# Kernel optimization log

Hardware: AMD Instinct MI355X
Metric: run time of the kernel (lower is better)

Reference implementation:

```python
import jax, jax.numpy as jnp
import numpy as np

N, E, B = 100000, 1200000, 512
IN_DIM, HID, K, NCLS = 64, 64, 3, 10


def setup_inputs() -> dict:
    key = jax.random.key(0)
    ks = jax.random.split(key, 10)
    features = jax.random.normal(ks[0], (N, IN_DIM), jnp.float32)
    edge_src = jax.random.randint(ks[1], (E,), 0, N)
    edge_dst = jax.random.randint(ks[2], (E,), 0, N)
    graph_ids = jnp.sort(jax.random.randint(ks[3], (N,), 0, B))
    s1 = float(1.0 / np.sqrt(IN_DIM))
    W1 = jax.random.uniform(ks[4], (IN_DIM, HID), jnp.float32, -s1, s1)
    b1 = jnp.zeros((HID,), jnp.float32)
    s2 = float(1.0 / np.sqrt(HID))
    W2 = jax.random.uniform(ks[5], (HID, HID), jnp.float32, -s2, s2)
    b2 = jnp.zeros((HID,), jnp.float32)
    s3 = float(1.0 / np.sqrt(HID * 3))
    cw = jax.random.uniform(ks[6], (HID, HID, 3), jnp.float32, -s3, s3)
    cb = jax.random.uniform(ks[7], (HID,), jnp.float32, -s3, s3)
    Wc = jax.random.uniform(ks[8], (HID, NCLS), jnp.float32, -s2, s2)
    bc = jax.random.uniform(ks[9], (NCLS,), jnp.float32, -s2, s2)
    return dict(features=features, edge_src=edge_src, edge_dst=edge_dst,
                graph_ids=graph_ids, num_graphs=B,
                W1=W1, b1=b1, W2=W2, b2=b2, cw=cw, cb=cb, Wc=Wc, bc=bc)


def graph_conv(h, src, dst, W, b, n_nodes):
    # DGL GraphConv, norm='both', allow_zero_in_degree (degrees clamped to 1)
    ones = jnp.ones((src.shape[0],), h.dtype)
    out_deg = jnp.zeros((n_nodes,), h.dtype).at[src].add(ones)
    in_deg = jnp.zeros((n_nodes,), h.dtype).at[dst].add(ones)
    norm_s = jax.lax.rsqrt(jnp.clip(out_deg, 1.0, None))
    norm_d = jax.lax.rsqrt(jnp.clip(in_deg, 1.0, None))
    m = (h * norm_s[:, None]) @ W  # weight first; math identical to agg-first
    agg = jnp.zeros((n_nodes, W.shape[1]), h.dtype).at[dst].add(m[src])
    return agg * norm_d[:, None] + b


def sort_pool(h, gid, num_graphs, k):
    # DGL SortPooling: sort each node's features ascending along feature dim,
    # then take top-k nodes per graph by last feature value (descending),
    # zero-padding graphs with < k nodes. Output [num_graphs, k*D].
    hs = jnp.sort(h, axis=-1)
    key = hs[:, -1]
    order = jnp.lexsort((-key, gid))  # gid asc, key desc
    gid_s = gid[order]
    hs_s = hs[order]
    n = gid.shape[0]
    start = jnp.full((num_graphs,), n).at[gid_s].min(jnp.arange(n))
    rank = jnp.arange(n) - start[gid_s]  # within-graph rank by key desc
    mask = rank < k
    slot = gid_s * k + jnp.clip(rank, 0, k - 1)
    out = jnp.zeros((num_graphs * k, hs.shape[-1]), h.dtype).at[slot].add(
        jnp.where(mask[:, None], hs_s, jnp.zeros((), h.dtype)))
    return out.reshape(num_graphs, k * hs.shape[-1])


def reference(features, edge_src, edge_dst, graph_ids, num_graphs,
              W1, b1, W2, b2, cw, cb, Wc, bc):
    n = features.shape[0]
    h = jax.nn.relu(graph_conv(features, edge_src, edge_dst, W1, b1, n))
    h = jax.nn.relu(graph_conv(h, edge_src, edge_dst, W2, b2, n))
    p = sort_pool(h, graph_ids, num_graphs, K)          # [B, K*HID]
    x = p.reshape(num_graphs, HID, K)                    # faithful torch reshape
    # Conv1d(kernel=3, stride=1) on length-3 input -> length-1 output
    y = jax.nn.relu(jnp.einsum('bct,oct->bo', x, cw) + cb)
    return y @ Wc + bc
```

## Files before the change

kernel.cpp:

```cpp
#include <hip/hip_runtime.h>
#include <hip/hip_bf16.h>


#define PART_H 50176
#define QPART_H (PART_H / 4)
#define PART_F 25088
#define QUART_F (PART_F / 4)
#define MCH  64

__global__ void __launch_bounds__(256) k_histgemm(
    const int* __restrict__ esrc, const int* __restrict__ edst,
    unsigned char* __restrict__ hd, unsigned char* __restrict__ hs,
    const float* __restrict__ in, const float* __restrict__ W,
    float* __restrict__ mout, int N, int E, int PH, int histBlocks) {
  __shared__ float smem[12800];
  const int t = threadIdx.x;
  if (blockIdx.x < histBlocks) {
    unsigned int* lc = (unsigned int*)smem;
    const int b = blockIdx.x;
    const int half = PH * MCH;
    const int a = b / half;
    const int r = b % half;
    const int p = r % PH;
    const int m = r / PH;
    const int* __restrict__ arr = a ? esrc : edst;
    unsigned char* __restrict__ outp = a ? hs : hd;
    const int base = p * PART_H;
    const int lim = min(PART_H, N - base);
    for (int i = t; i < QPART_H; i += 256) lc[i] = 0u;
    __syncthreads();
    const long long cb = (long long)m * E / MCH;
    const long long ce = (long long)(m + 1) * E / MCH;
    const long long a0 = min((cb + 3) & ~3LL, ce);
    const long long nv = (ce - a0) >> 2;
    for (long long e = cb + t; e < a0; e += 256) {
      int d = arr[e] - base;
      if ((unsigned)d < (unsigned)lim) atomicAdd(&lc[d >> 2], 1u << ((d & 3) * 8));
    }
    const int4* __restrict__ a4p = (const int4*)(arr + a0);
    for (long long i = t; i < nv; i += 256) {
      int4 v4 = a4p[i];
      int d;
      d = v4.x - base; if ((unsigned)d < (unsigned)lim) atomicAdd(&lc[d >> 2], 1u << ((d & 3) * 8));
      d = v4.y - base; if ((unsigned)d < (unsigned)lim) atomicAdd(&lc[d >> 2], 1u << ((d & 3) * 8));
      d = v4.z - base; if ((unsigned)d < (unsigned)lim) atomicAdd(&lc[d >> 2], 1u << ((d & 3) * 8));
      d = v4.w - base; if ((unsigned)d < (unsigned)lim) atomicAdd(&lc[d >> 2], 1u << ((d & 3) * 8));
    }
    for (long long e = a0 + (nv << 2) + t; e < ce; e += 256) {
      int d = arr[e] - base;
      if ((unsigned)d < (unsigned)lim) atomicAdd(&lc[d >> 2], 1u << ((d & 3) * 8));
    }
    __syncthreads();
    unsigned char* slice = outp + ((size_t)p * MCH + m) * PART_H;
    for (int i = t; i < lim; i += 256)
      slice[i] = (unsigned char)((lc[i >> 2] >> ((i & 3) * 8)) & 0xffu);
  } else {
    float* Wl = smem;
    float* Ac = smem + 4096;
    const int ch = (t & 7) * 8;
    const int nb = (t >> 3) * 4;
    for (int i = t; i < 1024; i += 256)
      ((float4*)Wl)[i] = ((const float4*)W)[i];
    const int gb = blockIdx.x - histBlocks;
    const int ng = gridDim.x - histBlocks;
    const int NT = (N + 127) >> 7;
    for (int tile = gb; tile < NT; tile += ng) {
      const int vbase = tile << 7;
      __syncthreads();
      for (int i = t; i < 2048; i += 256) {
        const int r = i >> 4;
        const int c = (i & 15) * 4;
        const int v = vbase + r;
        float4 val = make_float4(0.f, 0.f, 0.f, 0.f);
        if (v < N) val = *(const float4*)(in + (size_t)v * 64 + c);
        Ac[(c + 0) * 136 + r] = val.x;
        Ac[(c + 1) * 136 + r] = val.y;
        Ac[(c + 2) * 136 + r] = val.z;
        Ac[(c + 3) * 136 + r] = val.w;
      }
      __syncthreads();
      float acc[4][8];
#pragma unroll
      for (int j = 0; j < 4; ++j)
#pragma unroll
        for (int c = 0; c < 8; ++c) acc[j][c] = 0.f;
      for (int k = 0; k < 64; k += 4) {
#pragma unroll
        for (int kk = 0; kk < 4; ++kk) {
          const float4 aa = *(const float4*)&Ac[(k + kk) * 136 + nb];
          const float4 w0 = *(const float4*)&Wl[(k + kk) * 64 + ch];
          const float4 w1 = *(const float4*)&Wl[(k + kk) * 64 + ch + 4];
          const float an[4] = {aa.x, aa.y, aa.z, aa.w};
          const float wn[8] = {w0.x, w0.y, w0.z, w0.w, w1.x, w1.y, w1.z, w1.w};
#pragma unroll
          for (int j = 0; j < 4; ++j)
#pragma unroll
            for (int c = 0; c < 8; ++c)
              acc[j][c] = fmaf(an[j], wn[c], acc[j][c]);
        }
      }
#pragma unroll
      for (int j = 0; j < 4; ++j) {
        const int v = vbase + nb + j;
        if (v < N) {
          float4 o0, o1;
          o0.x = acc[j][0]; o0.y = acc[j][1]; o0.z = acc[j][2]; o0.w = acc[j][3];
          o1.x = acc[j][4]; o1.y = acc[j][5]; o1.z = acc[j][6]; o1.w = acc[j][7];
          *(float4*)(mout + (size_t)v * 64 + ch)     = o0;
          *(float4*)(mout + (size_t)v * 64 + ch + 4) = o1;
        }
      }
    }
  }
}

__global__ void __launch_bounds__(256) k_offscan(
    unsigned char* __restrict__ hd, const unsigned char* __restrict__ hs,
    int* __restrict__ deg_d, float* __restrict__ norm_s, float* __restrict__ norm_d,
    int* __restrict__ gstart, int* __restrict__ rowptr, int* __restrict__ bsum,
    int B, int N) {
  __shared__ int sums[256];
  const int t = threadIdx.x;
  const int v0 = blockIdx.x * 2048 + t * 8;
#pragma unroll
  for (int j = 0; j < 8; ++j)
    if (v0 + j < B) gstart[v0 + j] = 0x7f7f7f7f;
  unsigned long long drun = 0ull, stot = 0ull;
  if (v0 < N) {
    const size_t rb = (size_t)(v0 / PART_H) * MCH * PART_H + (size_t)(v0 % PART_H);
    unsigned long long* __restrict__ hd8 = (unsigned long long*)(hd + rb);
    const unsigned long long* __restrict__ hs8 = (const unsigned long long*)(hs + rb);
    const size_t st8 = PART_H / 8;
#pragma unroll 8
    for (int m = 0; m < MCH; ++m) {
      unsigned long long c = hd8[(size_t)m * st8];
      hd8[(size_t)m * st8] = drun;
      drun += c;
      stot += hs8[(size_t)m * st8];
    }
  }
  int loc[8];
  int tot = 0;
#pragma unroll
  for (int j = 0; j < 8; ++j) {
    const int v = v0 + j;
    const int dg = (v < N) ? (int)((drun >> (8 * j)) & 0xffull) : 0;
    loc[j] = tot;
    tot += dg;
    if (v < N) {
      deg_d[v] = dg;
      norm_d[v] = rsqrtf((float)max(dg, 1));
      const int so = (int)((stot >> (8 * j)) & 0xffull);
      norm_s[v] = rsqrtf((float)max(so, 1));
    }
  }
  sums[t] = tot;
  __syncthreads();
  for (int off = 1; off < 256; off <<= 1) {
    int x = (t >= off) ? sums[t - off] : 0;
    __syncthreads();
    sums[t] += x;
    __syncthreads();
  }
  int excl = (t == 0) ? 0 : sums[t - 1];
#pragma unroll
  for (int j = 0; j < 8; ++j) {
    const int v = v0 + j;
    if (v < N) rowptr[v] = excl + loc[j];
  }
  if (t == 255) bsum[blockIdx.x] = sums[255];
}

__global__ void k_scan2(int* __restrict__ bsum, int nb) {
  int lane = threadIdx.x;
  int v = (lane < nb) ? bsum[lane] : 0;
  int inc = v;
#pragma unroll
  for (int off = 1; off < 64; off <<= 1) {
    int o = __shfl_up(inc, off, 64);
    if (lane >= off) inc += o;
  }
  if (lane < nb) bsum[lane] = inc - v;
}

__global__ void k_fill2(const int* __restrict__ esrc, const int* __restrict__ edst,
                        const unsigned char* __restrict__ hd, const int* __restrict__ rowptr,
                        const int* __restrict__ bsum, int* __restrict__ csr,
                        int N, int E, int PF) {
  __shared__ unsigned int cur4[QUART_F];
  const int b = blockIdx.x;
  const int p = b % PF;
  const int m = b / PF;
  const int base = p * PART_F;
  const int lim = min(PART_F, N - base);
  const unsigned char* slice = hd + ((size_t)(p >> 1) * MCH + m) * PART_H
                                  + (size_t)(p & 1) * PART_F;
  const unsigned int* slice4 = (const unsigned int*)slice;
  for (int i = threadIdx.x; i < QUART_F; i += blockDim.x) cur4[i] = slice4[i];
  __syncthreads();
  const int* __restrict__ rp = rowptr + base;
  const long long cb = (long long)m * E / MCH;
  const long long ce = (long long)(m + 1) * E / MCH;
  const long long a0 = min((cb + 3) & ~3LL, ce);
  const long long nv = (ce - a0) >> 2;
  for (long long e = cb + threadIdx.x; e < a0; e += blockDim.x) {
    int d = edst[e] - base;
    if ((unsigned)d < (unsigned)lim) {
      unsigned int old = atomicAdd(&cur4[d >> 2], 1u << ((d & 3) * 8));
      csr[rp[d] + bsum[(base + d) >> 11] + ((old >> ((d & 3) * 8)) & 0xff)] = esrc[e];
    }
  }
  const int4* __restrict__ d4p = (const int4*)(edst + a0);
  const int4* __restrict__ s4p = (const int4*)(esrc + a0);
  for (long long i = threadIdx.x; i < nv; i += blockDim.x) {
    int4 d4 = d4p[i];
    int4 s4 = s4p[i];
    int d;
    d = d4.x - base;
    if ((unsigned)d < (unsigned)lim) {
      unsigned int old = atomicAdd(&cur4[d >> 2], 1u << ((d & 3) * 8));
      csr[rp[d] + bsum[(base + d) >> 11] + ((old >> ((d & 3) * 8)) & 0xff)] = s4.x;
    }
    d = d4.y - base;
    if ((unsigned)d < (unsigned)lim) {
      unsigned int old = atomicAdd(&cur4[d >> 2], 1u << ((d & 3) * 8));
      csr[rp[d] + bsum[(base + d) >> 11] + ((old >> ((d & 3) * 8)) & 0xff)] = s4.y;
    }
    d = d4.z - base;
    if ((unsigned)d < (unsigned)lim) {
      unsigned int old = atomicAdd(&cur4[d >> 2], 1u << ((d & 3) * 8));
      csr[rp[d] + bsum[(base + d) >> 11] + ((old >> ((d & 3) * 8)) & 0xff)] = s4.z;
    }
    d = d4.w - base;
    if ((unsigned)d < (unsigned)lim) {
      unsigned int old = atomicAdd(&cur4[d >> 2], 1u << ((d & 3) * 8));
      csr[rp[d] + bsum[(base + d) >> 11] + ((old >> ((d & 3) * 8)) & 0xff)] = s4.w;
    }
  }
  for (long long e = a0 + (nv << 2) + threadIdx.x; e < ce; e += blockDim.x) {
    int d = edst[e] - base;
    if ((unsigned)d < (unsigned)lim) {
      unsigned int old = atomicAdd(&cur4[d >> 2], 1u << ((d & 3) * 8));
      csr[rp[d] + bsum[(base + d) >> 11] + ((old >> ((d & 3) * 8)) & 0xff)] = esrc[e];
    }
  }
}

__global__ void __launch_bounds__(256) k_gemm64(
    const float* __restrict__ in, const float* __restrict__ norm,
    const float* __restrict__ W, float* __restrict__ out, int N) {
  __shared__ float Wl[4096];
  __shared__ float Ac[64 * 136];
  const int t = threadIdx.x;
  const int ch = (t & 7) * 8;
  const int nb = (t >> 3) * 4;
  for (int i = t; i < 1024; i += 256)
    ((float4*)Wl)[i] = ((const float4*)W)[i];
  const int NT = (N + 127) >> 7;
  for (int tile = blockIdx.x; tile < NT; tile += gridDim.x) {
    const int vbase = tile << 7;
    __syncthreads();
    for (int i = t; i < 2048; i += 256) {
      const int r = i >> 4;
      const int c = (i & 15) * 4;
      const int v = vbase + r;
      float4 val = make_float4(0.f, 0.f, 0.f, 0.f);
      if (v < N) val = *(const float4*)(in + (size_t)v * 64 + c);
      Ac[(c + 0) * 136 + r] = val.x;
      Ac[(c + 1) * 136 + r] = val.y;
      Ac[(c + 2) * 136 + r] = val.z;
      Ac[(c + 3) * 136 + r] = val.w;
    }
    __syncthreads();
    float acc[4][8];
#pragma unroll
    for (int j = 0; j < 4; ++j)
#pragma unroll
      for (int c = 0; c < 8; ++c) acc[j][c] = 0.f;
    for (int k = 0; k < 64; k += 4) {
#pragma unroll
      for (int kk = 0; kk < 4; ++kk) {
        const float4 aa = *(const float4*)&Ac[(k + kk) * 136 + nb];
        const float4 w0 = *(const float4*)&Wl[(k + kk) * 64 + ch];
        const float4 w1 = *(const float4*)&Wl[(k + kk) * 64 + ch + 4];
        const float an[4] = {aa.x, aa.y, aa.z, aa.w};
        const float wn[8] = {w0.x, w0.y, w0.z, w0.w, w1.x, w1.y, w1.z, w1.w};
#pragma unroll
        for (int j = 0; j < 4; ++j)
#pragma unroll
          for (int c = 0; c < 8; ++c)
            acc[j][c] = fmaf(an[j], wn[c], acc[j][c]);
      }
    }
#pragma unroll
    for (int j = 0; j < 4; ++j) {
      const int v = vbase + nb + j;
      if (v < N) {
        const float nm = norm[v];
        float4 o0, o1;
        o0.x = acc[j][0] * nm; o0.y = acc[j][1] * nm;
        o0.z = acc[j][2] * nm; o0.w = acc[j][3] * nm;
        o1.x = acc[j][4] * nm; o1.y = acc[j][5] * nm;
        o1.z = acc[j][6] * nm; o1.w = acc[j][7] * nm;
        *(float4*)(out + (size_t)v * 64 + ch)     = o0;
        *(float4*)(out + (size_t)v * 64 + ch + 4) = o1;
      }
    }
  }
}

__global__ void k_gather(const float* __restrict__ m, const int* __restrict__ rowptr,
                         const int* __restrict__ bsum,
                         const int* __restrict__ deg, const float* __restrict__ norm_d,
                         const float* __restrict__ bias, const int* __restrict__ csr,
                         const float* __restrict__ nsrc,
                         const int* __restrict__ gid, int* __restrict__ gstart,
                         float* __restrict__ h, float* __restrict__ key, int N) {
  const int wpb = blockDim.x >> 6;
  const int nwaves = gridDim.x * wpb;
  const int lane = threadIdx.x & 63;
  const int chb = (lane & 7) * 8;
  const int grp = lane >> 3;
  const float4 b0 = *(const float4*)(bias + chb);
  const float4 b1 = *(const float4*)(bias + chb + 4);
  for (int w = blockIdx.x * wpb + (threadIdx.x >> 6); w < N; w += nwaves) {
    if (gid != nullptr && lane == 0) {
      int g = gid[w];
      if (w == 0 || gid[w - 1] != g) gstart[g] = w;
    }
    const int start = rowptr[w] + bsum[w >> 11];
    const int cnt = deg[w];
    float4 a00 = make_float4(0.f, 0.f, 0.f, 0.f);
    float4 a01 = make_float4(0.f, 0.f, 0.f, 0.f);
    float4 a10 = make_float4(0.f, 0.f, 0.f, 0.f);
    float4 a11 = make_float4(0.f, 0.f, 0.f, 0.f);
    int i = grp;
    if (nsrc != nullptr) {
      for (; i + 8 < cnt; i += 16) {
        int s0 = csr[start + i];
        int s1 = csr[start + i + 8];
        float n0 = nsrc[s0], n1 = nsrc[s1];
        const float* r0 = m + (size_t)s0 * 64 + chb;
        const float* r1 = m + (size_t)s1 * 64 + chb;
        const float4 v00 = *(const float4*)r0;
        const float4 v01 = *(const float4*)(r0 + 4);
        const float4 v10 = *(const float4*)r1;
        const float4 v11 = *(const float4*)(r1 + 4);
        a00.x = fmaf(v00.x, n0, a00.x); a00.y = fmaf(v00.y, n0, a00.y);
        a00.z = fmaf(v00.z, n0, a00.z); a00.w = fmaf(v00.w, n0, a00.w);
        a01.x = fmaf(v01.x, n0, a01.x); a01.y = fmaf(v01.y, n0, a01.y);
        a01.z = fmaf(v01.z, n0, a01.z); a01.w = fmaf(v01.w, n0, a01.w);
        a10.x = fmaf(v10.x, n1, a10.x); a10.y = fmaf(v10.y, n1, a10.y);
        a10.z = fmaf(v10.z, n1, a10.z); a10.w = fmaf(v10.w, n1, a10.w);
        a11.x = fmaf(v11.x, n1, a11.x); a11.y = fmaf(v11.y, n1, a11.y);
        a11.z = fmaf(v11.z, n1, a11.z); a11.w = fmaf(v11.w, n1, a11.w);
      }
      if (i < cnt) {
        int s0 = csr[start + i];
        float n0 = nsrc[s0];
        const float* r0 = m + (size_t)s0 * 64 + chb;
        const float4 v00 = *(const float4*)r0;
        const float4 v01 = *(const float4*)(r0 + 4);
        a00.x = fmaf(v00.x, n0, a00.x); a00.y = fmaf(v00.y, n0, a00.y);
        a00.z = fmaf(v00.z, n0, a00.z); a00.w = fmaf(v00.w, n0, a00.w);
        a01.x = fmaf(v01.x, n0, a01.x); a01.y = fmaf(v01.y, n0, a01.y);
        a01.z = fmaf(v01.z, n0, a01.z); a01.w = fmaf(v01.w, n0, a01.w);
      }
    } else {
      for (; i + 8 < cnt; i += 16) {
        int s0 = csr[start + i];
        int s1 = csr[start + i + 8];
        const float* r0 = m + (size_t)s0 * 64 + chb;
        const float* r1 = m + (size_t)s1 * 64 + chb;
        const float4 v00 = *(const float4*)r0;
        const float4 v01 = *(const float4*)(r0 + 4);
        const float4 v10 = *(const float4*)r1;
        const float4 v11 = *(const float4*)(r1 + 4);
        a00.x += v00.x; a00.y += v00.y; a00.z += v00.z; a00.w += v00.w;
        a01.x += v01.x; a01.y += v01.y; a01.z += v01.z; a01.w += v01.w;
        a10.x += v10.x; a10.y += v10.y; a10.z += v10.z; a10.w += v10.w;
        a11.x += v11.x; a11.y += v11.y; a11.z += v11.z; a11.w += v11.w;
      }
      if (i < cnt) {
        int s0 = csr[start + i];
        const float* r0 = m + (size_t)s0 * 64 + chb;
        const float4 v00 = *(const float4*)r0;
        const float4 v01 = *(const float4*)(r0 + 4);
        a00.x += v00.x; a00.y += v00.y; a00.z += v00.z; a00.w += v00.w;
        a01.x += v01.x; a01.y += v01.y; a01.z += v01.z; a01.w += v01.w;
      }
    }
    a00.x += a10.x; a00.y += a10.y; a00.z += a10.z; a00.w += a10.w;
    a01.x += a11.x; a01.y += a11.y; a01.z += a11.z; a01.w += a11.w;
#pragma unroll
    for (int off = 8; off <= 32; off <<= 1) {
      a00.x += __shfl_xor(a00.x, off, 64);
      a00.y += __shfl_xor(a00.y, off, 64);
      a00.z += __shfl_xor(a00.z, off, 64);
      a00.w += __shfl_xor(a00.w, off, 64);
      a01.x += __shfl_xor(a01.x, off, 64);
      a01.y += __shfl_xor(a01.y, off, 64);
      a01.z += __shfl_xor(a01.z, off, 64);
      a01.w += __shfl_xor(a01.w, off, 64);
    }
    const float nd = norm_d[w];
    float4 o0, o1;
    o0.x = fmaxf(fmaf(a00.x, nd, b0.x), 0.f);
    o0.y = fmaxf(fmaf(a00.y, nd, b0.y), 0.f);
    o0.z = fmaxf(fmaf(a00.z, nd, b0.z), 0.f);
    o0.w = fmaxf(fmaf(a00.w, nd, b0.w), 0.f);
    o1.x = fmaxf(fmaf(a01.x, nd, b1.x), 0.f);
    o1.y = fmaxf(fmaf(a01.y, nd, b1.y), 0.f);
    o1.z = fmaxf(fmaf(a01.z, nd, b1.z), 0.f);
    o1.w = fmaxf(fmaf(a01.w, nd, b1.w), 0.f);
    if (grp == 0) {
      *(float4*)(h + (size_t)w * 64 + chb)     = o0;
      *(float4*)(h + (size_t)w * 64 + chb + 4) = o1;
    }
    if (key != nullptr) {
      float mx = fmaxf(fmaxf(fmaxf(o0.x, o0.y), fmaxf(o0.z, o0.w)),
                       fmaxf(fmaxf(o1.x, o1.y), fmaxf(o1.z, o1.w)));
#pragma unroll
      for (int off = 1; off < 8; off <<= 1) mx = fmaxf(mx, __shfl_xor(mx, off, 64));
      if (lane == 0) key[w] = mx;
    }
  }
}

__global__ void __launch_bounds__(256) k_tail(
    const float* __restrict__ key, const int* __restrict__ gstart,
    const float* __restrict__ h,
    const float* __restrict__ cw, const float* __restrict__ cb,
    const float* __restrict__ Wc, const float* __restrict__ bc,
    float* __restrict__ out, int B, int N) {
  __shared__ int sel[3];
  __shared__ float prow[192];
  const int b = blockIdx.x;
  const int wid = threadIdx.x >> 6;
  const int lane = threadIdx.x & 63;

  if (wid == 0) {
    const int gs = gstart[b];
    int g2 = b + 1;
    while (g2 < B && gstart[g2] >= N) ++g2;
    const int ns = (g2 < B) ? gstart[g2] : N;
    const int s = gs;
    const int c = (gs < N) ? (ns - gs) : 0;
    float v0 = -1.f, v1 = -1.f, v2 = -1.f;
    int i0 = 0x7fffffff, i1 = 0x7fffffff, i2 = 0x7fffffff;
    for (int i = s + lane; i < s + c; i += 64) {
      float kv = key[i];
      if (kv > v0 || (kv == v0 && i < i0)) {
        v2 = v1; i2 = i1; v1 = v0; i1 = i0; v0 = kv; i0 = i;
      } else if (kv > v1 || (kv == v1 && i < i1)) {
        v2 = v1; i2 = i1; v1 = kv; i1 = i;
      } else if (kv > v2 || (kv == v2 && i < i2)) {
        v2 = kv; i2 = i;
      }
    }
    int ptr = 0;
    for (int r = 0; r < 3; ++r) {
      float mv = (ptr == 0) ? v0 : (ptr == 1) ? v1 : (ptr == 2) ? v2 : -1.f;
      int   mi = (ptr == 0) ? i0 : (ptr == 1) ? i1 : (ptr == 2) ? i2 : 0x7fffffff;
      float bv = mv; int bi = mi;
#pragma unroll
      for (int off = 32; off; off >>= 1) {
        float ov = __shfl_xor(bv, off, 64);
        int   oi = __shfl_xor(bi, off, 64);
        if (ov > bv || (ov == bv && oi < bi)) { bv = ov; bi = oi; }
      }
      if (bi == mi && ptr < 3) ptr++;
      if (lane == 0) sel[r] = (bi == 0x7fffffff) ? -1 : bi;
    }
  }
  __syncthreads();
  if (wid < 3) {
    int node = sel[wid];
    float v = 0.f;
    if (node >= 0) {
      v = h[(size_t)node * 64 + lane];
      for (int k2 = 2; k2 <= 64; k2 <<= 1) {
        for (int j = k2 >> 1; j > 0; j >>= 1) {
          float o = __shfl_xor(v, j, 64);
          bool up = ((lane & k2) == 0);
          bool lower = ((lane & j) == 0);
          v = (lower == up) ? fminf(v, o) : fmaxf(v, o);
        }
      }
    }
    prow[wid * 64 + lane] = v;
  }
  __syncthreads();
  if (wid == 0) {
    float y = cb[lane];
    for (int j = 0; j < 192; ++j) y = fmaf(prow[j], cw[lane * 192 + j], y);
    float ry = fmaxf(y, 0.f);
    for (int c = 0; c < 10; ++c) {
      float s = ry * Wc[lane * 10 + c];
#pragma unroll
      for (int off = 32; off; off >>= 1) s += __shfl_xor(s, off, 64);
      if (lane == 0) out[b * 10 + c] = s + bc[c];
    }
  }
}

extern "C" void kernel_launch(void* const* d_in, const int* in_sizes, int n_in,
                              void* d_out, int out_size, void* d_ws, size_t ws_size,
                              hipStream_t stream) {
  const float* features = (const float*)d_in[0];
  const int*   esrc     = (const int*)d_in[1];
  const int*   edst     = (const int*)d_in[2];
  const int*   gid      = (const int*)d_in[3];
  const float* W1 = (const float*)d_in[5];
  const float* b1 = (const float*)d_in[6];
  const float* W2 = (const float*)d_in[7];
  const float* b2 = (const float*)d_in[8];
  const float* cw = (const float*)d_in[9];
  const float* cb = (const float*)d_in[10];
  const float* Wc = (const float*)d_in[11];
  const float* bc = (const float*)d_in[12];
  float* out = (float*)d_out;

  const int N = in_sizes[0] / 64;
  const int E = in_sizes[1];
  const int B = out_size / 10;
  const size_t N64 = (size_t)N * 64;
  const int nscan = (N + 2047) / 2048;
  const int PH = (N + PART_H - 1) / PART_H;
  const int PF = (N + PART_F - 1) / PART_F;
  const size_t HSZ = (size_t)PH * MCH * PART_H;
  const int NT = (N + 127) / 128;
  const int histBlocks = 2 * PH * MCH;

  float* bufA   = (float*)d_ws;
  float* bufB   = bufA + N64;
  int*   deg_d  = (int*)(bufB + N64);
  float* norm_s = (float*)(deg_d + N);
  float* norm_d = norm_s + N;
  float* key    = norm_d + N;
  int*   rowptr = (int*)(key + N);
  int*   csr    = rowptr + N;
  int*   bsum   = csr + E;
  int*   gstart = bsum + 64;
  unsigned char* hd = (unsigned char*)(((size_t)(gstart + B) + 15) & ~(size_t)15);
  unsigned char* hs = hd + HSZ;

  const int TB = 256;

  k_histgemm<<<histBlocks + NT, TB, 0, stream>>>(esrc, edst, hd, hs,
                                                 features, W1, bufA,
                                                 N, E, PH, histBlocks);
  k_offscan<<<nscan, 256, 0, stream>>>(hd, hs, deg_d, norm_s, norm_d,
                                       gstart, rowptr, bsum, B, N);
  k_scan2<<<1, 64, 0, stream>>>(bsum, nscan);
  k_fill2<<<PF * MCH, TB, 0, stream>>>(esrc, edst, hd, rowptr, bsum, csr, N, E, PF);

  const int GB = 2048;

  k_gather<<<GB, TB, 0, stream>>>(bufA, rowptr, bsum, deg_d, norm_d, b1,
                                  csr, norm_s, nullptr, nullptr,
                                  bufB, nullptr, N);

  k_gemm64<<<NT, TB, 0, stream>>>(bufB, norm_s, W2, bufA, N);
  k_gather<<<GB, TB, 0, stream>>>(bufA, rowptr, bsum, deg_d, norm_d, b2,
                                  csr, nullptr, gid, gstart,
                                  bufB, key, N);

  k_tail<<<B, TB, 0, stream>>>(key, gstart, bufB, cw, cb, Wc, bc, out, B, N);
}
```

Before: 329.5 us.

## Parallelize offset scan across more blocks by splitting chunk scan among threads

Rebuilds the degree/offset scan so each block covers 256 nodes instead of 2048. The 64 histogram chunks per 8-node group are split across 8 threads, with partial sums combined in shared memory. This gives far more blocks and shorter serial loops, aiming to cut the latency of a kernel that previously ran on few blocks. In exchange the block-sum scan becomes a 512-thread shared-memory scan, and every consumer indexes bsum at 256-node granularity.

```diff
diff --git a/kernel.cpp b/kernel.cpp
--- a/kernel.cpp
+++ b/kernel.cpp
@@ -119,42 +119,62 @@
     int* __restrict__ deg_d, float* __restrict__ norm_s, float* __restrict__ norm_d,
     int* __restrict__ gstart, int* __restrict__ rowptr, int* __restrict__ bsum,
     int B, int N) {
+  __shared__ unsigned long long part[32][8];
+  __shared__ unsigned long long spart[32][8];
   __shared__ int sums[256];
   const int t = threadIdx.x;
-  const int v0 = blockIdx.x * 2048 + t * 8;
-#pragma unroll
-  for (int j = 0; j < 8; ++j)
-    if (v0 + j < B) gstart[v0 + j] = 0x7f7f7f7f;
-  unsigned long long drun = 0ull, stot = 0ull;
-  if (v0 < N) {
-    const size_t rb = (size_t)(v0 / PART_H) * MCH * PART_H + (size_t)(v0 % PART_H);
-    unsigned long long* __restrict__ hd8 = (unsigned long long*)(hd + rb);
-    const unsigned long long* __restrict__ hs8 = (const unsigned long long*)(hs + rb);
-    const size_t st8 = PART_H / 8;
-#pragma unroll 8
-    for (int m = 0; m < MCH; ++m) {
-      unsigned long long c = hd8[(size_t)m * st8];
-      hd8[(size_t)m * st8] = drun;
-      drun += c;
-      stot += hs8[(size_t)m * st8];
-    }
-  }
-  int loc[8];
-  int tot = 0;
-#pragma unroll
-  for (int j = 0; j < 8; ++j) {
-    const int v = v0 + j;
-    const int dg = (v < N) ? (int)((drun >> (8 * j)) & 0xffull) : 0;
-    loc[j] = tot;
-    tot += dg;
-    if (v < N) {
-      deg_d[v] = dg;
-      norm_d[v] = rsqrtf((float)max(dg, 1));
-      const int so = (int)((stot >> (8 * j)) & 0xffull);
-      norm_s[v] = rsqrtf((float)max(so, 1));
-    }
-  }
-  sums[t] = tot;
+  const int s = t >> 3;
+  const int c = t & 7;
+  const int nb0 = blockIdx.x * 256;
+  const int v0 = nb0 + s * 8;
+  const int vt = nb0 + t;
+  if (vt < B) gstart[vt] = 0x7f7f7f7f;
+  const size_t rb = (size_t)(v0 / PART_H) * MCH * PART_H + (size_t)(v0 % PART_H);
+  unsigned long long* __restrict__ hd8 = (unsigned long long*)(hd + rb);
+  const unsigned long long* __restrict__ hs8 = (const unsigned long long*)(hs + rb);
+  const size_t st8 = PART_H / 8;
+  const int m0 = c * 8;
+  const bool act = (v0 < N);
+  unsigned long long vals[8];
+  unsigned long long tsum = 0ull, hsum = 0ull;
+  if (act) {
+#pragma unroll
+    for (int k = 0; k < 8; ++k) {
+      vals[k] = hd8[(size_t)(m0 + k) * st8];
+      tsum += vals[k];
+      hsum += hs8[(size_t)(m0 + k) * st8];
+    }
+  }
+  part[s][c] = tsum;
+  spart[s][c] = hsum;
+  __syncthreads();
+  if (act) {
+    unsigned long long run = 0ull;
+#pragma unroll
+    for (int cc = 0; cc < 8; ++cc)
+      if (cc < c) run += part[s][cc];
+#pragma unroll
+    for (int k = 0; k < 8; ++k) {
+      const unsigned long long w = vals[k];
+      hd8[(size_t)(m0 + k) * st8] = run;
+      run += w;
+    }
+  }
+  unsigned long long dt = 0ull, ht = 0ull;
+#pragma unroll
+  for (int cc = 0; cc < 8; ++cc) {
+    dt += part[t >> 3][cc];
+    ht += spart[t >> 3][cc];
+  }
+  int dg = 0;
+  if (vt < N) {
+    dg = (int)((dt >> (8 * (t & 7))) & 0xffull);
+    const int so = (int)((ht >> (8 * (t & 7))) & 0xffull);
+    deg_d[vt] = dg;
+    norm_d[vt] = rsqrtf((float)max(dg, 1));
+    norm_s[vt] = rsqrtf((float)max(so, 1));
+  }
+  sums[t] = dg;
   __syncthreads();
   for (int off = 1; off < 256; off <<= 1) {
     int x = (t >= off) ? sums[t - off] : 0;
@@ -162,25 +182,23 @@
     sums[t] += x;
     __syncthreads();
   }
-  int excl = (t == 0) ? 0 : sums[t - 1];
-#pragma unroll
-  for (int j = 0; j < 8; ++j) {
-    const int v = v0 + j;
-    if (v < N) rowptr[v] = excl + loc[j];
-  }
+  if (vt < N) rowptr[vt] = sums[t] - dg;
   if (t == 255) bsum[blockIdx.x] = sums[255];
 }
 
 __global__ void k_scan2(int* __restrict__ bsum, int nb) {
-  int lane = threadIdx.x;
-  int v = (lane < nb) ? bsum[lane] : 0;
-  int inc = v;
-#pragma unroll
-  for (int off = 1; off < 64; off <<= 1) {
-    int o = __shfl_up(inc, off, 64);
-    if (lane >= off) inc += o;
-  }
-  if (lane < nb) bsum[lane] = inc - v;
+  __shared__ int sh[512];
+  const int t = threadIdx.x;
+  const int v = (t < nb) ? bsum[t] : 0;
+  sh[t] = v;
+  __syncthreads();
+  for (int off = 1; off < 512; off <<= 1) {
+    int x = (t >= off) ? sh[t - off] : 0;
+    __syncthreads();
+    sh[t] += x;
+    __syncthreads();
+  }
+  if (t < nb) bsum[t] = sh[t] - v;
 }
 
 __global__ void k_fill2(const int* __restrict__ esrc, const int* __restrict__ edst,
@@ -207,7 +225,7 @@
     int d = edst[e] - base;
     if ((unsigned)d < (unsigned)lim) {
       unsigned int old = atomicAdd(&cur4[d >> 2], 1u << ((d & 3) * 8));
-      csr[rp[d] + bsum[(base + d) >> 11] + ((old >> ((d & 3) * 8)) & 0xff)] = esrc[e];
+      csr[rp[d] + bsum[(base + d) >> 8] + ((old >> ((d & 3) * 8)) & 0xff)] = esrc[e];
     }
   }
   const int4* __restrict__ d4p = (const int4*)(edst + a0);
@@ -219,29 +237,29 @@
     d = d4.x - base;
     if ((unsigned)d < (unsigned)lim) {
       unsigned int old = atomicAdd(&cur4[d >> 2], 1u << ((d & 3) * 8));
-      csr[rp[d] + bsum[(base + d) >> 11] + ((old >> ((d & 3) * 8)) & 0xff)] = s4.x;
+      csr[rp[d] + bsum[(base + d) >> 8] + ((old >> ((d & 3) * 8)) & 0xff)] = s4.x;
     }
     d = d4.y - base;
     if ((unsigned)d < (unsigned)lim) {
       unsigned int old = atomicAdd(&cur4[d >> 2], 1u << ((d & 3) * 8));
-      csr[rp[d] + bsum[(base + d) >> 11] + ((old >> ((d & 3) * 8)) & 0xff)] = s4.y;
+      csr[rp[d] + bsum[(base + d) >> 8] + ((old >> ((d & 3) * 8)) & 0xff)] = s4.y;
     }
     d = d4.z - base;
     if ((unsigned)d < (unsigned)lim) {
       unsigned int old = atomicAdd(&cur4[d >> 2], 1u << ((d & 3) * 8));
-      csr[rp[d] + bsum[(base + d) >> 11] + ((old >> ((d & 3) * 8)) & 0xff)] = s4.z;
+      csr[rp[d] + bsum[(base + d) >> 8] + ((old >> ((d & 3) * 8)) & 0xff)] = s4.z;
     }
     d = d4.w - base;
     if ((unsigned)d < (unsigned)lim) {
       unsigned int old = atomicAdd(&cur4[d >> 2], 1u << ((d & 3) * 8));
-      csr[rp[d] + bsum[(base + d) >> 11] + ((old >> ((d & 3) * 8)) & 0xff)] = s4.w;
+      csr[rp[d] + bsum[(base + d) >> 8] + ((old >> ((d & 3) * 8)) & 0xff)] = s4.w;
     }
   }
   for (long long e = a0 + (nv << 2) + threadIdx.x; e < ce; e += blockDim.x) {
     int d = edst[e] - base;
     if ((unsigned)d < (unsigned)lim) {
       unsigned int old = atomicAdd(&cur4[d >> 2], 1u << ((d & 3) * 8));
-      csr[rp[d] + bsum[(base + d) >> 11] + ((old >> ((d & 3) * 8)) & 0xff)] = esrc[e];
+      csr[rp[d] + bsum[(base + d) >> 8] + ((old >> ((d & 3) * 8)) & 0xff)] = esrc[e];
     }
   }
 }
@@ -328,7 +346,7 @@
       int g = gid[w];
       if (w == 0 || gid[w - 1] != g) gstart[g] = w;
     }
-    const int start = rowptr[w] + bsum[w >> 11];
+    const int start = rowptr[w] + bsum[w >> 8];
     const int cnt = deg[w];
     float4 a00 = make_float4(0.f, 0.f, 0.f, 0.f);
     float4 a01 = make_float4(0.f, 0.f, 0.f, 0.f);
@@ -525,7 +543,7 @@
   const int E = in_sizes[1];
   const int B = out_size / 10;
   const size_t N64 = (size_t)N * 64;
-  const int nscan = (N + 2047) / 2048;
+  const int nscan = (N + 255) / 256;
   const int PH = (N + PART_H - 1) / PART_H;
   const int PF = (N + PART_F - 1) / PART_F;
   const size_t HSZ = (size_t)PH * MCH * PART_H;
@@ -541,7 +559,7 @@
   int*   rowptr = (int*)(key + N);
   int*   csr    = rowptr + N;
   int*   bsum   = csr + E;
-  int*   gstart = bsum + 64;
+  int*   gstart = bsum + 512;
   unsigned char* hd = (unsigned char*)(((size_t)(gstart + B) + 15) & ~(size_t)15);
   unsigned char* hs = hd + HSZ;
 
@@ -552,7 +570,7 @@
                                                  N, E, PH, histBlocks);
   k_offscan<<<nscan, 256, 0, stream>>>(hd, hs, deg_d, norm_s, norm_d,
                                        gstart, rowptr, bsum, B, N);
-  k_scan2<<<1, 64, 0, stream>>>(bsum, nscan);
+  k_scan2<<<1, 512, 0, stream>>>(bsum, nscan);
   k_fill2<<<PF * MCH, TB, 0, stream>>>(esrc, edst, hd, rowptr, bsum, csr, N, E, PF);
 
   const int GB = 2048;
```

After: 294.2 us. 10.7% less time.
